# Kernel optimization log

Hardware: AMD Instinct MI355X
Metric: run time of the kernel (lower is better)

The kernel has to match this reference:

```python
import jax, jax.numpy as jnp
import numpy as np

NEG_INF = -9e15  # matches torch reference mask value
LEAKY_SLOPE = 0.2  # alpha passed to nn.LeakyReLU


def setup_inputs() -> dict:
    key = jax.random.key(0)
    k1, k2, k3 = jax.random.split(key, 3)
    B, N, E = 256, 300, 100
    item_embeddings = jax.random.normal(k1, (B, N, E), dtype=jnp.float32)
    adj = jax.random.randint(k2, (B, N, N), 0, 5, dtype=jnp.int64)  # edge types 0..4
    A = jax.random.normal(k3, (4, E), dtype=jnp.float32)  # stacked a_0..a_3
    return {"item_embeddings": item_embeddings, "adj": adj, "A": A}


def reference(item_embeddings, adj, A):
    h = item_embeddings  # [B, N, E]
    # Original: a_input[b,i,j,:] = h[b,i,:] * h[b,j,:]; e_k = leakyrelu(a_input @ a_k).
    # Equivalent without the (B,N,N,E) tensor: e_k[b,i,j] = lrelu(sum_d h[b,i,d] h[b,j,d] A[k,d]).
    e = jnp.einsum('bid,bjd,kd->kbij', h, h, A)  # [4, B, N, N]
    e = jax.nn.leaky_relu(e, LEAKY_SLOPE)
    mask = jnp.full_like(e[0], NEG_INF)
    alpha = jnp.where(adj == 1, e[0], mask)
    alpha = jnp.where(adj == 2, e[1], alpha)
    alpha = jnp.where(adj == 3, e[2], alpha)
    alpha = jnp.where(adj == 4, e[3], alpha)
    alpha = jax.nn.softmax(alpha, axis=-1)
    return jnp.matmul(alpha, h)  # [B, N, E]
```

## Files before the change

kernel.cpp:

```cpp
#include <hip/hip_runtime.h>


typedef _Float16 half8 __attribute__((ext_vector_type(8)));
typedef _Float16 half4 __attribute__((ext_vector_type(4)));
typedef float f32x4 __attribute__((ext_vector_type(4)));

constexpr int B_ = 256, N_ = 300, E_ = 100;
constexpr float NEGINF = -9e15f;
constexpr float PADV   = -3e38f;
constexpr float LOG2E  = 1.44269504088896f;

constexpr int PART_OFF  = 69120;
constexpr int LDS_BYTES = 69120 + 9 * 7680;

#define TRD(dst, addr, off) \
  asm volatile("ds_read_b64_tr_b16 %0, %1 offset:" #off : "=v"(dst) : "v"(addr))
#define LGKM0 do { asm volatile("s_waitcnt lgkmcnt(0)" ::: "memory"); \
                   __builtin_amdgcn_sched_barrier(0); } while (0)

__global__ __launch_bounds__(1024)
void gat_flash14(const float* __restrict__ H, const int* __restrict__ ADJ,
                 const float* __restrict__ A, float* __restrict__ OUT) {
  extern __shared__ char smraw[];
  _Float16* hS   = (_Float16*)smraw;
  _Float16* A16  = (_Float16*)(smraw + 68096);
  float*    part = (float*)(smraw + PART_OFF);

  const int b = blockIdx.x;
  const int tid = threadIdx.x;
  const int w = tid >> 6, lane = tid & 63;
  const int lg = lane >> 4, ll = lane & 15;

  const float* Hb  = H + (size_t)b * (N_ * E_);
  const int*   AJb = ADJ + (size_t)b * (N_ * N_);

  for (int u = tid; u < 304 * 14; u += 1024) {
    const int j = u / 14, hr = u % 14;
    half8 v;
#pragma unroll
    for (int e = 0; e < 8; ++e) {
      const int d = hr * 8 + e;
      v[e] = (_Float16)((j < N_ && d < E_) ? Hb[j * E_ + d] : 0.f);
    }
    *(half8*)&hS[(((j >> 4) * 7 + (hr >> 1)) << 8) + ((j & 15) << 4) + ((hr & 1) << 3)] = v;
  }
  if (tid < 64) {
    const int k = tid >> 4, oct = tid & 15;
    half8 v;
#pragma unroll
    for (int e = 0; e < 8; ++e) {
      const int d = oct * 8 + e;
      v[e] = (_Float16)((d < E_) ? A[k * E_ + d] * LOG2E : 0.f);
    }
    *(half8*)&A16[k * 128 + oct * 8] = v;
  }
  __syncthreads();

  const unsigned ldsbase = (unsigned)(size_t)(void*)hS;
  const unsigned trlane  = (unsigned)(ll * 8 + lg * 128);

  half8 g[3][4];
  half4 gt[4];
  float m, lsum;
  f32x4 acc[7];
  const int* ajrow = AJb;

  auto prep_strip = [&](int s) {
    const int irow = s * 16 + ll;
    const int irc  = irow < N_ ? irow : N_ - 1;
    ajrow = AJb + (size_t)irc * N_;
#pragma unroll
    for (int db = 0; db < 3; ++db) {
      const int doct = db * 4 + lg;
      const half8 hi = *(const half8*)&hS[((s * 7 + (doct >> 1)) << 8) + (ll << 4) + ((doct & 1) << 3)];
#pragma unroll
      for (int k = 0; k < 4; ++k)
        g[db][k] = hi * *(const half8*)&A16[k * 128 + doct * 8];
    }
    const half4 hit = *(const half4*)&hS[((s * 7 + 6) << 8) + (ll << 4) + lg * 4];
#pragma unroll
    for (int k = 0; k < 4; ++k)
      gt[k] = hit * *(const half4*)&A16[k * 128 + 96 + lg * 4];
    m = PADV; lsum = 0.f;
#pragma unroll
    for (int t = 0; t < 7; ++t) acc[t] = (f32x4){0.f, 0.f, 0.f, 0.f};
  };

  auto load_adj = [&](int jt) -> int4 {
    int jc = jt * 16 + lg * 4;
    if (jc > N_ - 4) jc = N_ - 4;
    return *(const int4*)(ajrow + jc);
  };

  auto tile_body = [&](int jt, int4 av, bool tail) {
    f32x4 c0 = {0.f, 0.f, 0.f, 0.f}, c1 = c0, c2 = c0, c3 = c0;
#pragma unroll
    for (int db = 0; db < 3; ++db) {
      const int doct = db * 4 + lg;
      const half8 aj = *(const half8*)&hS[((jt * 7 + (doct >> 1)) << 8) + (ll << 4) + ((doct & 1) << 3)];
      c0 = __builtin_amdgcn_mfma_f32_16x16x32_f16(aj, g[db][0], c0, 0, 0, 0);
      c1 = __builtin_amdgcn_mfma_f32_16x16x32_f16(aj, g[db][1], c1, 0, 0, 0);
      c2 = __builtin_amdgcn_mfma_f32_16x16x32_f16(aj, g[db][2], c2, 0, 0, 0);
      c3 = __builtin_amdgcn_mfma_f32_16x16x32_f16(aj, g[db][3], c3, 0, 0, 0);
    }
    {
      const half4 ajt = *(const half4*)&hS[((jt * 7 + 6) << 8) + (ll << 4) + lg * 4];
      c0 = __builtin_amdgcn_mfma_f32_16x16x16f16(ajt, gt[0], c0, 0, 0, 0);
      c1 = __builtin_amdgcn_mfma_f32_16x16x16f16(ajt, gt[1], c1, 0, 0, 0);
      c2 = __builtin_amdgcn_mfma_f32_16x16x16f16(ajt, gt[2], c2, 0, 0, 0);
      c3 = __builtin_amdgcn_mfma_f32_16x16x16f16(ajt, gt[3], c3, 0, 0, 0);
    }
    const int va[4] = {av.x, av.y, av.z, av.w};
    float sv[4];
#pragma unroll
    for (int r = 0; r < 4; ++r) {
      const float e = (va[r] == 1) ? c0[r] : (va[r] == 2) ? c1[r]
                     : (va[r] == 3) ? c2[r] : c3[r];
      sv[r] = (va[r] == 0) ? NEGINF : fmaxf(e, 0.2f * e);
    }
    if (tail && lg == 3) { sv[0] = PADV; sv[1] = PADV; sv[2] = PADV; sv[3] = PADV; }

    const unsigned trb = ldsbase + (unsigned)(jt * 3584) + trlane;
    half4 tr[7];
    TRD(tr[0], trb, 0);    TRD(tr[1], trb, 512);  TRD(tr[2], trb, 1024);
    TRD(tr[3], trb, 1536); TRD(tr[4], trb, 2048); TRD(tr[5], trb, 2560);
    TRD(tr[6], trb, 3072);

    const float lmax = fmaxf(fmaxf(sv[0], sv[1]), fmaxf(sv[2], sv[3]));
    if (__any(lmax > m + 8.f)) {
      float tmax = fmaxf(lmax, __shfl_xor(lmax, 16));
      tmax = fmaxf(tmax, __shfl_xor(tmax, 32));
      const float nm = fmaxf(m, tmax);
      const float f = exp2f(m - nm);
      m = nm; lsum *= f;
#pragma unroll
      for (int t = 0; t < 7; ++t) {
        acc[t][0] *= f; acc[t][1] *= f; acc[t][2] *= f; acc[t][3] *= f;
      }
    }
    const float p0 = exp2f(sv[0] - m), p1 = exp2f(sv[1] - m);
    const float p2 = exp2f(sv[2] - m), p3 = exp2f(sv[3] - m);
    lsum += (p0 + p1) + (p2 + p3);
    half4 pb;
    pb[0] = (_Float16)p0; pb[1] = (_Float16)p1;
    pb[2] = (_Float16)p2; pb[3] = (_Float16)p3;

    LGKM0;
#pragma unroll
    for (int t = 0; t < 7; ++t)
      acc[t] = __builtin_amdgcn_mfma_f32_16x16x16f16(tr[t], pb, acc[t], 0, 0, 0);
  };

  auto store_rows = [&](int s) {
    lsum += __shfl_xor(lsum, 16);
    lsum += __shfl_xor(lsum, 32);
    const float rv = 1.f / lsum;
    const int irow = s * 16 + ll;
    if (irow < N_) {
      float* orow = OUT + ((size_t)b * N_ + irow) * E_;
#pragma unroll
      for (int t = 0; t < 7; ++t) {
        const int e0 = t * 16 + lg * 4;
        if (e0 < E_) {
          f32x4 o = acc[t];
          o[0] *= rv; o[1] *= rv; o[2] *= rv; o[3] *= rv;
          *(f32x4*)&orow[e0] = o;
        }
      }
    }
  };

  prep_strip(w);
  {
    int4 av = load_adj(0);
    for (int jt = 0; jt < 18; ++jt) {
      const int4 nv = load_adj(jt + 1);
      tile_body(jt, av, false);
      av = nv;
    }
    tile_body(18, av, true);
  }
  store_rows(w);

  if (w < 12) {
    const int t = w >> 2, q = w & 3;
    const int s2 = 16 + t;
    prep_strip(s2);
    const int j0 = q * 5;
    const int j1 = (q < 3) ? (j0 + 5) : 18;
    int4 av = load_adj(j0);
    for (int jt = j0; jt < j1; ++jt) {
      const int4 nv = load_adj(jt + 1);
      tile_body(jt, av, false);
      av = nv;
    }
    if (q == 3) tile_body(18, av, true);

    if (q) {
      float* dst = part + (size_t)(t * 3 + (q - 1)) * 1920 + lane * 30;
#pragma unroll
      for (int tt = 0; tt < 7; ++tt) {
        dst[4 * tt + 0] = acc[tt][0]; dst[4 * tt + 1] = acc[tt][1];
        dst[4 * tt + 2] = acc[tt][2]; dst[4 * tt + 3] = acc[tt][3];
      }
      dst[28] = m; dst[29] = lsum;
    }
  }
  __syncthreads();

  if (w < 12 && (w & 3) == 0) {
    const int t = w >> 2;
#pragma unroll
    for (int q = 1; q <= 3; ++q) {
      const float* src = part + (size_t)(t * 3 + (q - 1)) * 1920 + lane * 30;
      const float mq = src[28], lq = src[29];
      const float M  = fmaxf(m, mq);
      const float f0 = exp2f(m - M), f1 = exp2f(mq - M);
      m = M;
      lsum = lsum * f0 + lq * f1;
#pragma unroll
      for (int tt = 0; tt < 7; ++tt) {
        acc[tt][0] = acc[tt][0] * f0 + src[4 * tt + 0] * f1;
        acc[tt][1] = acc[tt][1] * f0 + src[4 * tt + 1] * f1;
        acc[tt][2] = acc[tt][2] * f0 + src[4 * tt + 2] * f1;
        acc[tt][3] = acc[tt][3] * f0 + src[4 * tt + 3] * f1;
      }
    }
    store_rows(16 + t);
  }
}

extern "C" void kernel_launch(void* const* d_in, const int* in_sizes, int n_in,
                              void* d_out, int out_size, void* d_ws, size_t ws_size,
                              hipStream_t stream) {
  const float* H  = (const float*)d_in[0];
  const int*   AJ = (const int*)d_in[1];
  const float* A  = (const float*)d_in[2];
  float* OUT = (float*)d_out;

  (void)hipFuncSetAttribute(reinterpret_cast<const void*>(gat_flash14),
                            hipFuncAttributeMaxDynamicSharedMemorySize,
                            LDS_BYTES);
  gat_flash14<<<B_, 1024, LDS_BYTES, stream>>>(H, AJ, A, OUT);
}
```

Baseline: 83.28 us.

## Rebalance strip-tile work evenly across 12 waves with split-softmax merging

Reduces the block from 16 to 12 waves and gives each wave a contiguous range of 30 (strip, key-tile) units out of 361 total, so every wave does nearly equal work. Previously 16 waves each did a full strip and then 12 waves split the remaining 3 strips. A wave whose range begins mid-strip writes partial flash-softmax state to LDS, and the wave holding the start of that strip merges it after a barrier. This removes the tail imbalance of the second phase, at the cost of fewer waves to hide latency and more LDS for partials.

```diff
diff --git a/kernel.cpp b/kernel.cpp
--- a/kernel.cpp
+++ b/kernel.cpp
@@ -11,15 +11,15 @@
 constexpr float LOG2E  = 1.44269504088896f;
 
 constexpr int PART_OFF  = 69120;
-constexpr int LDS_BYTES = 69120 + 9 * 7680;
+constexpr int LDS_BYTES = 69120 + 11 * 7680;
 
 #define TRD(dst, addr, off) \
   asm volatile("ds_read_b64_tr_b16 %0, %1 offset:" #off : "=v"(dst) : "v"(addr))
 #define LGKM0 do { asm volatile("s_waitcnt lgkmcnt(0)" ::: "memory"); \
                    __builtin_amdgcn_sched_barrier(0); } while (0)
 
-__global__ __launch_bounds__(1024)
-void gat_flash14(const float* __restrict__ H, const int* __restrict__ ADJ,
+__global__ __launch_bounds__(768)
+void gat_flash16(const float* __restrict__ H, const int* __restrict__ ADJ,
                  const float* __restrict__ A, float* __restrict__ OUT) {
   extern __shared__ char smraw[];
   _Float16* hS   = (_Float16*)smraw;
@@ -34,7 +34,7 @@
   const float* Hb  = H + (size_t)b * (N_ * E_);
   const int*   AJb = ADJ + (size_t)b * (N_ * N_);
 
-  for (int u = tid; u < 304 * 14; u += 1024) {
+  for (int u = tid; u < 304 * 14; u += 768) {
     const int j = u / 14, hr = u % 14;
     half8 v;
 #pragma unroll
@@ -152,9 +152,10 @@
   };
 
   auto store_rows = [&](int s) {
-    lsum += __shfl_xor(lsum, 16);
-    lsum += __shfl_xor(lsum, 32);
-    const float rv = 1.f / lsum;
+    float ls = lsum;
+    ls += __shfl_xor(ls, 16);
+    ls += __shfl_xor(ls, 32);
+    const float rv = 1.f / ls;
     const int irow = s * 16 + ll;
     if (irow < N_) {
       float* orow = OUT + ((size_t)b * N_ + irow) * E_;
@@ -170,63 +171,55 @@
     }
   };
 
-  prep_strip(w);
-  {
-    int4 av = load_adj(0);
-    for (int jt = 0; jt < 18; ++jt) {
-      const int4 nv = load_adj(jt + 1);
-      tile_body(jt, av, false);
-      av = nv;
-    }
-    tile_body(18, av, true);
-  }
-  store_rows(w);
-
-  if (w < 12) {
-    const int t = w >> 2, q = w & 3;
-    const int s2 = 16 + t;
-    prep_strip(s2);
-    const int j0 = q * 5;
-    const int j1 = (q < 3) ? (j0 + 5) : 18;
+  int u = 30 * w;
+  const int u1 = (w == 11) ? 361 : (u + 30);
+  bool held = false;
+  int s_held = 0;
+
+  while (u < u1) {
+    const int s  = u / 19;
+    const int j0 = u - 19 * s;
+    const int j1 = (19 < j0 + (u1 - u)) ? 19 : (j0 + (u1 - u));
+    prep_strip(s);
     int4 av = load_adj(j0);
     for (int jt = j0; jt < j1; ++jt) {
-      const int4 nv = load_adj(jt + 1);
-      tile_body(jt, av, false);
+      const int4 nv = (jt + 1 < j1) ? load_adj(jt + 1) : av;
+      tile_body(jt, av, jt == 18);
       av = nv;
     }
-    if (q == 3) tile_body(18, av, true);
-
-    if (q) {
-      float* dst = part + (size_t)(t * 3 + (q - 1)) * 1920 + lane * 30;
-#pragma unroll
-      for (int tt = 0; tt < 7; ++tt) {
-        dst[4 * tt + 0] = acc[tt][0]; dst[4 * tt + 1] = acc[tt][1];
-        dst[4 * tt + 2] = acc[tt][2]; dst[4 * tt + 3] = acc[tt][3];
+    if (j0 > 0) {
+      float* dst = part + (size_t)(w - 1) * 1920 + lane * 30;
+#pragma unroll
+      for (int t = 0; t < 7; ++t) {
+        dst[4 * t + 0] = acc[t][0]; dst[4 * t + 1] = acc[t][1];
+        dst[4 * t + 2] = acc[t][2]; dst[4 * t + 3] = acc[t][3];
       }
       dst[28] = m; dst[29] = lsum;
-    }
-  }
+    } else if (j1 < 19) {
+      held = true; s_held = s;
+    } else {
+      store_rows(s);
+    }
+    u += j1 - j0;
+  }
+
   __syncthreads();
 
-  if (w < 12 && (w & 3) == 0) {
-    const int t = w >> 2;
-#pragma unroll
-    for (int q = 1; q <= 3; ++q) {
-      const float* src = part + (size_t)(t * 3 + (q - 1)) * 1920 + lane * 30;
-      const float mq = src[28], lq = src[29];
-      const float M  = fmaxf(m, mq);
-      const float f0 = exp2f(m - M), f1 = exp2f(mq - M);
-      m = M;
-      lsum = lsum * f0 + lq * f1;
-#pragma unroll
-      for (int tt = 0; tt < 7; ++tt) {
-        acc[tt][0] = acc[tt][0] * f0 + src[4 * tt + 0] * f1;
-        acc[tt][1] = acc[tt][1] * f0 + src[4 * tt + 1] * f1;
-        acc[tt][2] = acc[tt][2] * f0 + src[4 * tt + 2] * f1;
-        acc[tt][3] = acc[tt][3] * f0 + src[4 * tt + 3] * f1;
-      }
-    }
-    store_rows(16 + t);
+  if (held) {
+    const float* src = part + (size_t)w * 1920 + lane * 30;
+    const float mq = src[28], lq = src[29];
+    const float M  = fmaxf(m, mq);
+    const float f0 = exp2f(m - M), f1 = exp2f(mq - M);
+    m = M;
+    lsum = lsum * f0 + lq * f1;
+#pragma unroll
+    for (int t = 0; t < 7; ++t) {
+      acc[t][0] = acc[t][0] * f0 + src[4 * t + 0] * f1;
+      acc[t][1] = acc[t][1] * f0 + src[4 * t + 1] * f1;
+      acc[t][2] = acc[t][2] * f0 + src[4 * t + 2] * f1;
+      acc[t][3] = acc[t][3] * f0 + src[4 * t + 3] * f1;
+    }
+    store_rows(s_held);
   }
 }
 
@@ -238,8 +231,8 @@
   const float* A  = (const float*)d_in[2];
   float* OUT = (float*)d_out;
 
-  (void)hipFuncSetAttribute(reinterpret_cast<const void*>(gat_flash14),
+  (void)hipFuncSetAttribute(reinterpret_cast<const void*>(gat_flash16),
                             hipFuncAttributeMaxDynamicSharedMemorySize,
                             LDS_BYTES);
-  gat_flash14<<<B_, 1024, LDS_BYTES, stream>>>(H, AJ, A, OUT);
+  gat_flash16<<<B_, 768, LDS_BYTES, stream>>>(H, AJ, A, OUT);
 }
```

Measured after the change: 67.73 us. 18.7% less time.
